# Kernel tuning notes

Hardware: AMD Instinct MI355X
Metric: run time of the kernel (lower is better)

Reference implementation:

```python
import jax, jax.numpy as jnp
import numpy as np

NUM_HEADS = 12


def setup_inputs() -> dict:
    key = jax.random.key(0)
    k0, k1, k2 = jax.random.split(key, 3)
    B, S, D = 2, 2048, 1536
    scale = 1.0 / np.sqrt(D)
    return {
        "hidden_states": jax.random.normal(k0, (B, S, D), dtype=jnp.float32),
        "W_fc": jax.random.normal(k1, (D, D), dtype=jnp.float32) * scale,
        "b_fc": jnp.zeros((D,), dtype=jnp.float32),
        "W_proj": jax.random.normal(k2, (D, D), dtype=jnp.float32) * scale,
        "b_proj": jnp.zeros((D,), dtype=jnp.float32),
    }


def reference(hidden_states, W_fc, b_fc, W_proj, b_proj):
    B, S, D = hidden_states.shape
    H = NUM_HEADS
    hd = D // H
    # value_states: [B, H, S, hd] (key_states == value_states in the original)
    v = (hidden_states @ W_fc.T + b_fc).reshape(B, S, H, hd).transpose(0, 2, 1, 3)
    # Uniform-weight causal sliding-window attention, window_h = 2^(h+1)-1.
    i = jnp.arange(S)[:, None]          # query pos
    j = jnp.arange(S)[None, :]          # key pos
    w = (2 ** jnp.arange(1, H + 1, dtype=jnp.int32) - 1)[:, None, None]  # [H,1,1]
    mask = (j <= i) & (j >= i - w + 1)                                    # [H,S,S]
    valid_len = jnp.minimum(i + 1, w).astype(v.dtype)                     # [H,S,1]
    attn = jnp.where(mask, 1.0 / valid_len, 0.0)                          # [H,S,S]
    # [H,S,S] x [B,H,S,hd] -> [B,S,H,hd] -> [B,S,D]
    out = jnp.einsum("hqk,bhkd->bqhd", attn, v).reshape(B, S, D)
    attn_weights = jnp.broadcast_to(attn[None], (B, H, S, S))
    return out @ W_proj.T + b_proj, attn_weights
```

## Files before the change

kernel.cpp:

```cpp
#include <hip/hip_runtime.h>
#include <hip/hip_bf16.h>

#define S_LEN   2048
#define DMODEL  1536
#define NBATCH  2
#define NHEADS  12
#define MROWS   (NBATCH * S_LEN)
#define NCHUNK  16
#define CHUNK   128

typedef unsigned short u16;
typedef __attribute__((ext_vector_type(8))) short bf16x8;
typedef __attribute__((ext_vector_type(4))) float f32x4;

__device__ __forceinline__ u16 f2bf(float x) {
  unsigned u = __float_as_uint(x);
  u += 0x7fffu + ((u >> 16) & 1u);
  return (u16)(u >> 16);
}

#define N4_HID  1572864
#define N4_W    589824
__global__ void cvt_all(const float4* __restrict__ h, const float4* __restrict__ wf,
                        const float4* __restrict__ wp, ushort4* __restrict__ ho,
                        ushort4* __restrict__ wfo, ushort4* __restrict__ wpo) {
  int t = blockIdx.x * blockDim.x + threadIdx.x;
  const float4* src;
  ushort4* dst;
  int idx;
  if (t < N4_HID)            { src = h;  dst = ho;  idx = t; }
  else if (t < N4_HID + N4_W){ src = wf; dst = wfo; idx = t - N4_HID; }
  else                       { src = wp; dst = wpo; idx = t - N4_HID - N4_W; }
  float4 f = src[idx];
  ushort4 o;
  o.x = f2bf(f.x); o.y = f2bf(f.y); o.z = f2bf(f.z); o.w = f2bf(f.w);
  dst[idx] = o;
}

__device__ __forceinline__ void gld_lds16(u16* lds, const u16* g) {
  __builtin_amdgcn_global_load_lds(
      (const __attribute__((address_space(1))) unsigned int*)g,
      (__attribute__((address_space(3))) unsigned int*)lds, 16, 0, 0);
}

template <bool WITH_CSUM>
__global__ __launch_bounds__(256)
void gemm_bt_bias(const u16* __restrict__ A, const u16* __restrict__ B,
                  const float* __restrict__ bias, float* __restrict__ C,
                  float* __restrict__ cs, int Ndim, int Kdim) {
  __shared__ __align__(16) u16 As[128 * 32];
  __shared__ __align__(16) u16 Bs[128 * 32];
  __shared__ float colpart[2][128];

  const int tid  = threadIdx.x;
  const int wave = tid >> 6;
  const int lane = tid & 63;
  const int l15  = lane & 15;
  const int quad = lane >> 4;
  const int bm = blockIdx.y * 128;
  const int bn = blockIdx.x * 128;
  const int wm = (wave >> 1) * 64;
  const int wn = (wave & 1) * 64;

  f32x4 acc[4][4] = {};

  const int srow = wave * 32 + (lane >> 2);
  const int skk  = (lane & 3) * 8;
  const u16* gA = A + (size_t)(bm + srow) * Kdim + skk;
  const u16* gB = B + (size_t)(bn + srow) * Kdim + skk;
  u16* lA = &As[(wave * 32) * 32];
  u16* lB = &Bs[(wave * 32) * 32];
  const size_t rstep16 = (size_t)16 * Kdim;

  for (int k0 = 0; k0 < Kdim; k0 += 32) {
    gld_lds16(lA,           gA + k0);
    gld_lds16(lA + 16 * 32, gA + k0 + rstep16);
    gld_lds16(lB,           gB + k0);
    gld_lds16(lB + 16 * 32, gB + k0 + rstep16);
    __syncthreads();

    bf16x8 af[4], bfr[4];
#pragma unroll
    for (int i = 0; i < 4; ++i)
      af[i] = *(const bf16x8*)&As[(wm + i * 16 + l15) * 32 + quad * 8];
#pragma unroll
    for (int j = 0; j < 4; ++j)
      bfr[j] = *(const bf16x8*)&Bs[(wn + j * 16 + l15) * 32 + quad * 8];
#pragma unroll
    for (int i = 0; i < 4; ++i)
#pragma unroll
      for (int j = 0; j < 4; ++j)
        acc[i][j] = __builtin_amdgcn_mfma_f32_16x16x32_bf16(af[i], bfr[j], acc[i][j], 0, 0, 0);
    __syncthreads();
  }

  const int r0 = quad * 4;
#pragma unroll
  for (int j = 0; j < 4; ++j) {
    const int col = bn + wn + j * 16 + l15;
    const float bj = bias[col];
    float s = 0.f;
#pragma unroll
    for (int i = 0; i < 4; ++i) {
      const int row = bm + wm + i * 16 + r0;
#pragma unroll
      for (int r = 0; r < 4; ++r) {
        float cv = acc[i][j][r] + bj;
        C[(size_t)(row + r) * Ndim + col] = cv;
        s += cv;
      }
    }
    if (WITH_CSUM) {
      s += __shfl_xor(s, 16);
      s += __shfl_xor(s, 32);
      if (quad == 0) colpart[wm >> 6][wn + j * 16 + l15] = s;
    }
  }
  if (WITH_CSUM) {
    __syncthreads();
    if (tid < 128) {
      const int b = bm >> 11;
      const int c = (bm & 2047) >> 7;
      cs[((size_t)b * NCHUNK + c) * DMODEL + bn + tid] =
          colpart[0][tid] + colpart[1][tid];
    }
  }
}

__global__ void winavg_fused(const float* __restrict__ v, const float* __restrict__ cs,
                             u16* __restrict__ A2) {
  int t = blockIdx.x * blockDim.x + threadIdx.x;
  int d = t % DMODEL;
  int c = (t / DMODEL) % NCHUNK;
  int b = t / (DMODEL * NCHUNK);
  const int h = d >> 7;
  const int w = (2 << h) - 1;
  const float* vb = v + (size_t)b * S_LEN * DMODEL + d;
  const float* csb = cs + (size_t)b * NCHUNK * DMODEL + d;

  const int i0 = c * CHUNK;
  float lead = 0.f;
  for (int cc = 0; cc < c; ++cc) lead += csb[(size_t)cc * DMODEL];

  float trail = 0.f;
  const int tstart = i0 - w;
  if (tstart > 0) {
    const int tc = tstart >> 7;
    for (int cc = 0; cc < tc; ++cc) trail += csb[(size_t)cc * DMODEL];
#pragma unroll 4
    for (int r = tc * CHUNK; r < tstart; ++r) trail += vb[(size_t)r * DMODEL];
  }

  u16* out = A2 + ((size_t)(b * S_LEN + i0)) * DMODEL + d;
#pragma unroll 4
  for (int r = 0; r < CHUNK; ++r) {
    const int i = i0 + r;
    lead += vb[(size_t)i * DMODEL];
    float o;
    if (i < w) {
      o = lead / (float)(i + 1);
    } else {
      trail += vb[(size_t)(i - w) * DMODEL];
      o = (lead - trail) / (float)w;
    }
    out[(size_t)r * DMODEL] = f2bf(o);
  }
}

__global__ void attn_weights_kernel(float4* __restrict__ out4) {
  int t = blockIdx.x * blockDim.x + threadIdx.x;
  int j0 = (t & 511) << 2;
  int i  = (t >> 9) & (S_LEN - 1);
  int bh = t >> 20;
  int h  = bh >= NHEADS ? bh - NHEADS : bh;
  int w  = (2 << h) - 1;
  int len = min(i + 1, w);
  float inv = 1.0f / (float)len;
  int lo = i - w + 1;
  float4 r;
  r.x = (j0     <= i && j0     >= lo) ? inv : 0.f;
  r.y = (j0 + 1 <= i && j0 + 1 >= lo) ? inv : 0.f;
  r.z = (j0 + 2 <= i && j0 + 2 >= lo) ? inv : 0.f;
  r.w = (j0 + 3 <= i && j0 + 3 >= lo) ? inv : 0.f;
  out4[t] = r;
}

extern "C" void kernel_launch(void* const* d_in, const int* in_sizes, int n_in,
                              void* d_out, int out_size, void* d_ws, size_t ws_size,
                              hipStream_t stream) {
  const float* hidden = (const float*)d_in[0];
  const float* W_fc   = (const float*)d_in[1];
  const float* b_fc   = (const float*)d_in[2];
  const float* W_proj = (const float*)d_in[3];
  const float* b_proj = (const float*)d_in[4];
  float* outp = (float*)d_out;

  char* ws = (char*)d_ws;
  u16*   A16   = (u16*)(ws);
  u16*   Wfc16 = (u16*)(ws + 12582912);
  u16*   Wpj16 = (u16*)(ws + 17301504);
  float* vbuf  = (float*)(ws + 22020096);
  float* csums = (float*)(ws + 47185920);

  cvt_all<<<10752, 256, 0, stream>>>((const float4*)hidden, (const float4*)W_fc,
                                     (const float4*)W_proj, (ushort4*)A16,
                                     (ushort4*)Wfc16, (ushort4*)Wpj16);

  gemm_bt_bias<true><<<dim3(DMODEL / 128, MROWS / 128), 256, 0, stream>>>(
      A16, Wfc16, b_fc, vbuf, csums, DMODEL, DMODEL);

  winavg_fused<<<(NBATCH * NCHUNK * DMODEL) / 256, 256, 0, stream>>>(vbuf, csums, A16);

  gemm_bt_bias<false><<<dim3(DMODEL / 128, MROWS / 128), 256, 0, stream>>>(
      A16, Wpj16, b_proj, outp, nullptr, DMODEL, DMODEL);

  attn_weights_kernel<<<(NBATCH * NHEADS * S_LEN * S_LEN / 4) / 256, 256, 0, stream>>>(
      (float4*)(outp + (size_t)MROWS * DMODEL));
}
```

Before: 597.0 us.

## Store value projection in bf16 and use finer 32-row chunks for window sums

```diff
diff --git a/kernel.cpp b/kernel.cpp
--- a/kernel.cpp
+++ b/kernel.cpp
@@ -6,8 +6,8 @@
 #define NBATCH  2
 #define NHEADS  12
 #define MROWS   (NBATCH * S_LEN)
-#define NCHUNK  16
-#define CHUNK   128
+#define NCHUNK  64
+#define CHUNK   32
 
 typedef unsigned short u16;
 typedef __attribute__((ext_vector_type(8))) short bf16x8;
@@ -17,6 +17,9 @@
   unsigned u = __float_as_uint(x);
   u += 0x7fffu + ((u >> 16) & 1u);
   return (u16)(u >> 16);
+}
+__device__ __forceinline__ float bf2f(u16 x) {
+  return __uint_as_float(((unsigned)x) << 16);
 }
 
 #define N4_HID  1572864
@@ -43,14 +46,14 @@
       (__attribute__((address_space(3))) unsigned int*)lds, 16, 0, 0);
 }
 
-template <bool WITH_CSUM>
+template <bool WITH_CSUM, typename CT>
 __global__ __launch_bounds__(256)
 void gemm_bt_bias(const u16* __restrict__ A, const u16* __restrict__ B,
-                  const float* __restrict__ bias, float* __restrict__ C,
+                  const float* __restrict__ bias, CT* __restrict__ C,
                   float* __restrict__ cs, int Ndim, int Kdim) {
   __shared__ __align__(16) u16 As[128 * 32];
   __shared__ __align__(16) u16 Bs[128 * 32];
-  __shared__ float colpart[2][128];
+  __shared__ float colpart[4][128];
 
   const int tid  = threadIdx.x;
   const int wave = tid >> 6;
@@ -99,35 +102,42 @@
   for (int j = 0; j < 4; ++j) {
     const int col = bn + wn + j * 16 + l15;
     const float bj = bias[col];
-    float s = 0.f;
+    float sA = 0.f, sB = 0.f;
 #pragma unroll
     for (int i = 0; i < 4; ++i) {
       const int row = bm + wm + i * 16 + r0;
 #pragma unroll
       for (int r = 0; r < 4; ++r) {
         float cv = acc[i][j][r] + bj;
-        C[(size_t)(row + r) * Ndim + col] = cv;
-        s += cv;
+        if constexpr (sizeof(CT) == 2)
+          C[(size_t)(row + r) * Ndim + col] = (CT)f2bf(cv);
+        else
+          C[(size_t)(row + r) * Ndim + col] = (CT)cv;
+        if (WITH_CSUM) { if (i < 2) sA += cv; else sB += cv; }
       }
     }
     if (WITH_CSUM) {
-      s += __shfl_xor(s, 16);
-      s += __shfl_xor(s, 32);
-      if (quad == 0) colpart[wm >> 6][wn + j * 16 + l15] = s;
+      sA += __shfl_xor(sA, 16); sA += __shfl_xor(sA, 32);
+      sB += __shfl_xor(sB, 16); sB += __shfl_xor(sB, 32);
+      if (quad == 0) {
+        colpart[(wm >> 5) | 0][wn + j * 16 + l15] = sA;
+        colpart[(wm >> 5) | 1][wn + j * 16 + l15] = sB;
+      }
     }
   }
   if (WITH_CSUM) {
     __syncthreads();
     if (tid < 128) {
-      const int b = bm >> 11;
-      const int c = (bm & 2047) >> 7;
-      cs[((size_t)b * NCHUNK + c) * DMODEL + bn + tid] =
-          colpart[0][tid] + colpart[1][tid];
-    }
-  }
-}
-
-__global__ void winavg_fused(const float* __restrict__ v, const float* __restrict__ cs,
+      const int b  = bm >> 11;
+      const int c0 = (bm & 2047) >> 5;
+#pragma unroll
+      for (int g = 0; g < 4; ++g)
+        cs[((size_t)b * NCHUNK + c0 + g) * DMODEL + bn + tid] = colpart[g][tid];
+    }
+  }
+}
+
+__global__ void winavg_fused(const u16* __restrict__ v, const float* __restrict__ cs,
                              u16* __restrict__ A2) {
   int t = blockIdx.x * blockDim.x + threadIdx.x;
   int d = t % DMODEL;
@@ -135,7 +145,7 @@
   int b = t / (DMODEL * NCHUNK);
   const int h = d >> 7;
   const int w = (2 << h) - 1;
-  const float* vb = v + (size_t)b * S_LEN * DMODEL + d;
+  const u16* vb = v + (size_t)b * S_LEN * DMODEL + d;
   const float* csb = cs + (size_t)b * NCHUNK * DMODEL + d;
 
   const int i0 = c * CHUNK;
@@ -145,22 +155,22 @@
   float trail = 0.f;
   const int tstart = i0 - w;
   if (tstart > 0) {
-    const int tc = tstart >> 7;
+    const int tc = tstart >> 5;
     for (int cc = 0; cc < tc; ++cc) trail += csb[(size_t)cc * DMODEL];
 #pragma unroll 4
-    for (int r = tc * CHUNK; r < tstart; ++r) trail += vb[(size_t)r * DMODEL];
+    for (int r = tc * CHUNK; r < tstart; ++r) trail += bf2f(vb[(size_t)r * DMODEL]);
   }
 
   u16* out = A2 + ((size_t)(b * S_LEN + i0)) * DMODEL + d;
 #pragma unroll 4
   for (int r = 0; r < CHUNK; ++r) {
     const int i = i0 + r;
-    lead += vb[(size_t)i * DMODEL];
+    lead += bf2f(vb[(size_t)i * DMODEL]);
     float o;
     if (i < w) {
       o = lead / (float)(i + 1);
     } else {
-      trail += vb[(size_t)(i - w) * DMODEL];
+      trail += bf2f(vb[(size_t)(i - w) * DMODEL]);
       o = (lead - trail) / (float)w;
     }
     out[(size_t)r * DMODEL] = f2bf(o);
@@ -199,19 +209,19 @@
   u16*   A16   = (u16*)(ws);
   u16*   Wfc16 = (u16*)(ws + 12582912);
   u16*   Wpj16 = (u16*)(ws + 17301504);
-  float* vbuf  = (float*)(ws + 22020096);
-  float* csums = (float*)(ws + 47185920);
+  u16*   v16   = (u16*)(ws + 22020096);
+  float* csums = (float*)(ws + 34603008);
 
   cvt_all<<<10752, 256, 0, stream>>>((const float4*)hidden, (const float4*)W_fc,
                                      (const float4*)W_proj, (ushort4*)A16,
                                      (ushort4*)Wfc16, (ushort4*)Wpj16);
 
-  gemm_bt_bias<true><<<dim3(DMODEL / 128, MROWS / 128), 256, 0, stream>>>(
-      A16, Wfc16, b_fc, vbuf, csums, DMODEL, DMODEL);
-
-  winavg_fused<<<(NBATCH * NCHUNK * DMODEL) / 256, 256, 0, stream>>>(vbuf, csums, A16);
-
-  gemm_bt_bias<false><<<dim3(DMODEL / 128, MROWS / 128), 256, 0, stream>>>(
+  gemm_bt_bias<true, u16><<<dim3(DMODEL / 128, MROWS / 128), 256, 0, stream>>>(
+      A16, Wfc16, b_fc, v16, csums, DMODEL, DMODEL);
+
+  winavg_fused<<<(NBATCH * NCHUNK * DMODEL) / 256, 256, 0, stream>>>(v16, csums, A16);
+
+  gemm_bt_bias<false, float><<<dim3(DMODEL / 128, MROWS / 128), 256, 0, stream>>>(
       A16, Wpj16, b_proj, outp, nullptr, DMODEL, DMODEL);
 
   attn_weights_kernel<<<(NBATCH * NHEADS * S_LEN * S_LEN / 4) / 256, 256, 0, stream>>>(
```

New measurement: 567.9 us. 1.05x faster.
